# Kernel tuning notes

Hardware: AMD Instinct MI355X
Metric: run time of the kernel (lower is better)

Reference implementation:

```python
import jax, jax.numpy as jnp
import numpy as np

E, K, H, I = 16, 4, 2048, 1024
B, S = 1, 2048


def setup_inputs() -> dict:
    key = jax.random.key(0)
    ks = jax.random.split(key, 5)
    scale_in = 1.0 / np.sqrt(H)
    scale_mid = 1.0 / np.sqrt(I)
    return {
        "x": jax.random.normal(ks[0], (B, S, H), dtype=jnp.float32),
        "gate_w": jax.random.normal(ks[1], (E, H), dtype=jnp.float32) * scale_in,
        "w1_gate": jax.random.normal(ks[2], (E, I, H), dtype=jnp.float32) * scale_in,
        "w1_up": jax.random.normal(ks[3], (E, I, H), dtype=jnp.float32) * scale_in,
        "w2": jax.random.normal(ks[4], (E, H, I), dtype=jnp.float32) * scale_mid,
        "topk": K,
    }


def reference(x, gate_w, w1_gate, w1_up, w2, topk):
    orig_shape = x.shape
    xt = x.reshape(-1, x.shape[-1])            # [T, H]
    T = xt.shape[0]
    n_exp = gate_w.shape[0]

    # Router: top-k logits, softmax over the selected k (as in the torch code).
    logits = xt @ gate_w.T                      # [T, E]
    topk_vals, topk_ids = jax.lax.top_k(logits, topk)
    topk_w = jax.nn.softmax(topk_vals, axis=-1)  # [T, K]

    # Dense per-token-per-expert combine weight; 0 for unselected experts.
    # Mathematically identical to the gather/scatter-add loop: unselected
    # experts contribute expert_out * 0.
    gate_dense = jnp.zeros((T, n_exp), dtype=xt.dtype)
    gate_dense = gate_dense.at[jnp.arange(T)[:, None], topk_ids].add(topk_w)

    # SwiGLU per expert (dense over experts; weights zero-out unused ones).
    g = jnp.einsum("th,eih->tei", xt, w1_gate)   # [T, E, I]
    u = jnp.einsum("th,eih->tei", xt, w1_up)     # [T, E, I]
    h = jax.nn.silu(g) * u                        # [T, E, I]
    out = jnp.einsum("tei,te,ehi->th", h, gate_dense, w2)  # [T, H]
    return out.reshape(orig_shape)
```

## Files before the change

kernel.cpp:

```cpp
#include <hip/hip_runtime.h>
#include <hip/hip_bf16.h>
#include <stdint.h>

#define NEXP 16
#define KSEL 4
#define HDIM 2048
#define IDIM 1024
#define TTOK 2048
#define MAXTILES 80
#define NT1 16
#define NTB 16
#define MAXB1 (MAXTILES * NT1)
#define MAXBB (MAXTILES * NTB)
#define NCVT 1024
#define NW8 ((NEXP * IDIM * HDIM) / 8)

typedef __attribute__((ext_vector_type(8))) short bf16x8;
typedef __attribute__((ext_vector_type(4))) float f32x4;
typedef __attribute__((ext_vector_type(4))) unsigned int u32x4;
typedef unsigned int u32;

__device__ __forceinline__ uint32_t pack2(float a, float b) {
  __hip_bfloat162 h = __float22bfloat162_rn(float2{a, b});
  uint32_t u;
  __builtin_memcpy(&u, &h, 4);
  return u;
}
__device__ __forceinline__ ushort bf1(float a) {
  __hip_bfloat16 h = __float2bfloat16(a);
  ushort u;
  __builtin_memcpy(&u, &h, 2);
  return u;
}
__device__ __forceinline__ float bf2f(ushort u) {
  uint32_t v = (uint32_t)u << 16;
  float f;
  __builtin_memcpy(&f, &v, 4);
  return f;
}
__device__ __forceinline__ void gload16(const void* g, void* l) {
  __builtin_amdgcn_global_load_lds(
      (const __attribute__((address_space(1))) u32*)g,
      (__attribute__((address_space(3))) u32*)l, 16, 0, 0);
}
__device__ __forceinline__ int swzread(int row, int q) {
  return row * 32 + ((q ^ ((row >> 1) & 3)) << 3);
}
__device__ __forceinline__ void cvt_body(const float* __restrict__ src,
                                         ushort* __restrict__ dst,
                                         int blk, int nblk) {
  const int stride = nblk * 256;
  for (int i = blk * 256 + (int)threadIdx.x; i < NW8; i += stride) {
    f32x4 a = __builtin_nontemporal_load(((const f32x4*)src) + i * 2);
    f32x4 b = __builtin_nontemporal_load(((const f32x4*)src) + i * 2 + 1);
    uint4 t;
    t.x = pack2(a[0], a[1]); t.y = pack2(a[2], a[3]);
    t.z = pack2(b[0], b[1]); t.w = pack2(b[2], b[3]);
    ((uint4*)dst)[i] = t;
  }
}

__global__ __launch_bounds__(256) void router_kernel(
    const float* __restrict__ x, const float* __restrict__ gw,
    ushort* __restrict__ xb, int* __restrict__ topk_id,
    float* __restrict__ topk_w,
    const float* __restrict__ srcG, ushort* __restrict__ dstG,
    const float* __restrict__ srcU, ushort* __restrict__ dstU)
{
  if (blockIdx.x >= TTOK / 4 + NCVT) {
    cvt_body(srcU, dstU, blockIdx.x - (TTOK / 4 + NCVT), NCVT);
    return;
  }
  if (blockIdx.x >= TTOK / 4) {
    cvt_body(srcG, dstG, blockIdx.x - TTOK / 4, NCVT);
    return;
  }
  const int wid = threadIdx.x >> 6;
  const int lane = threadIdx.x & 63;
  const int t = blockIdx.x * 4 + wid;
  const float4* x4 = (const float4*)(x + (size_t)t * HDIM);
  const float4* gw4 = (const float4*)gw;
  float acc[NEXP];
#pragma unroll
  for (int e = 0; e < NEXP; ++e) acc[e] = 0.f;
#pragma unroll
  for (int i = 0; i < HDIM / 256; ++i) {
    const int idx = i * 64 + lane;
    float4 xv = x4[idx];
    uint2 xp;
    xp.x = pack2(xv.x, xv.y);
    xp.y = pack2(xv.z, xv.w);
    *(uint2*)(xb + (size_t)t * HDIM + idx * 4) = xp;
#pragma unroll
    for (int e = 0; e < NEXP; ++e) {
      float4 wv = gw4[e * (HDIM / 4) + idx];
      acc[e] += xv.x * wv.x + xv.y * wv.y + xv.z * wv.z + xv.w * wv.w;
    }
  }
#pragma unroll
  for (int e = 0; e < NEXP; ++e) {
#pragma unroll
    for (int off = 32; off >= 1; off >>= 1)
      acc[e] += __shfl_xor(acc[e], off);
  }
  if (lane == 0) {
    unsigned taken = 0;
    float vals[KSEL];
    int ids[KSEL];
#pragma unroll
    for (int k = 0; k < KSEL; ++k) {
      float bv = -3.4e38f; int bi = 0;
      for (int e = 0; e < NEXP; ++e)
        if (!((taken >> e) & 1u) && acc[e] > bv) { bv = acc[e]; bi = e; }
      taken |= 1u << bi; vals[k] = bv; ids[k] = bi;
    }
    float m = vals[0], s = 0.f, w[KSEL];
#pragma unroll
    for (int k = 0; k < KSEL; ++k) { w[k] = __expf(vals[k] - m); s += w[k]; }
    float is = 1.f / s;
#pragma unroll
    for (int k = 0; k < KSEL; ++k) {
      topk_id[t * KSEL + k] = ids[k];
      topk_w[t * KSEL + k] = w[k] * is;
    }
  }
}

__global__ __launch_bounds__(1024) void plan_scatter_kernel(
    const int* __restrict__ topk_id, int* __restrict__ counts,
    int* __restrict__ offsets, int* __restrict__ nWA, int* __restrict__ nWB,
    int* __restrict__ wlA, int* __restrict__ wlB,
    int* __restrict__ rowTok, int* __restrict__ inv)
{
  __shared__ int cnt[NEXP], off[NEXP], cur[NEXP], tiles[NEXP], pre[NEXP];
  const int tid = threadIdx.x;
  if (tid < NEXP) { cnt[tid] = 0; cur[tid] = 0; }
  __syncthreads();
  for (int i = tid; i < TTOK * KSEL; i += 1024)
    atomicAdd(&cnt[topk_id[i]], 1);
  __syncthreads();
  if (tid == 0) {
    int s = 0, p = 0;
    for (int e = 0; e < NEXP; ++e) {
      off[e] = s; s += cnt[e];
      tiles[e] = (cnt[e] + 127) >> 7;
      pre[e] = p; p += tiles[e];
    }
    *nWA = p * NT1;
    *nWB = p * NTB;
  }
  __syncthreads();
  if (tid < NEXP) {
    counts[tid] = cnt[tid];
    offsets[tid] = off[tid];
    const int e = tid, T = tiles[e];
    int idx = pre[e] * NT1;
    for (int nt = 0; nt < NT1; ++nt)
      for (int mt = 0; mt < T; ++mt)
        wlA[idx++] = (e << 12) | (nt << 6) | mt;
  } else if (tid < 2 * NEXP) {
    const int e = tid - NEXP, T = tiles[e];
    int idx = pre[e] * NTB;
    for (int nt = 0; nt < NTB; ++nt)
      for (int mt = 0; mt < T; ++mt)
        wlB[idx++] = (e << 12) | (nt << 6) | mt;
  }
  for (int i = tid; i < TTOK * KSEL; i += 1024) {
    const int e = topk_id[i];
    const int pos = atomicAdd(&cur[e], 1);
    const int row = off[e] + pos;
    rowTok[row] = i >> 2;
    inv[i] = row;
  }
}

__global__ __launch_bounds__(256) void gemm1_kernel(
    const ushort* __restrict__ xb,
    const ushort* __restrict__ wG, const ushort* __restrict__ wU,
    const int* __restrict__ rowTok, const int* __restrict__ counts,
    const int* __restrict__ offsets, const int* __restrict__ nW,
    const int* __restrict__ wl, ushort* __restrict__ hbuf,
    const float* __restrict__ cvsrc, ushort* __restrict__ cvdst)
{
  if (blockIdx.x >= MAXB1) {
    cvt_body(cvsrc, cvdst, blockIdx.x - MAXB1, NCVT);
    return;
  }
  const int nTot = *nW;
  const int L = (blockIdx.x & 7) * (MAXB1 / 8) + (blockIdx.x >> 3);
  if (L >= nTot) return;
  const int w = wl[L];
  const int e = w >> 12, nt = (w >> 6) & 63, mt = w & 63;
  const int n_e = counts[e], rowbase = offsets[e];

  __shared__ ushort As[2][128 * 32];
  __shared__ ushort Bg[2][64 * 32];
  __shared__ ushort Bu[2][64 * 32];

  const int tid = threadIdx.x;
  const int r0 = tid >> 2;
  const int ck = tid & 3;
  const int sch = (ck ^ ((r0 >> 1) & 3)) << 3;

  const int ar0 = mt * 128 + r0, ar1 = ar0 + 64;
  const int tok0 = rowTok[rowbase + (ar0 < n_e ? ar0 : n_e - 1)];
  const int tok1 = rowTok[rowbase + (ar1 < n_e ? ar1 : n_e - 1)];
  const ushort* pA0 = xb + (size_t)tok0 * HDIM + sch;
  const ushort* pA1 = xb + (size_t)tok1 * HDIM + sch;
  const size_t wbase = (size_t)e * IDIM * HDIM;
  const ushort* pBg = wG + wbase + (size_t)(nt * 64 + r0) * HDIM + sch;
  const ushort* pBu = wU + wbase + (size_t)(nt * 64 + r0) * HDIM + sch;

  const int lane = tid & 63;
  const int wid = tid >> 6;
  const int wr = (wid >> 1) << 6;
  const int wc = (wid & 1) << 5;
  const int lr = lane & 15;
  const int q = lane >> 4;

  f32x4 accG[4][2], accU[4][2];
#pragma unroll
  for (int i = 0; i < 4; ++i)
#pragma unroll
    for (int j = 0; j < 2; ++j) {
      accG[i][j] = (f32x4){0.f, 0.f, 0.f, 0.f};
      accU[i][j] = (f32x4){0.f, 0.f, 0.f, 0.f};
    }

  auto STAGE = [&](int b) {
    gload16(pA0, &As[b][tid * 8]);
    gload16(pA1, &As[b][2048 + tid * 8]);
    gload16(pBg, &Bg[b][tid * 8]);
    gload16(pBu, &Bu[b][tid * 8]);
    pA0 += 32; pA1 += 32; pBg += 32; pBu += 32;
  };

  const int NTK = HDIM / 32;
  STAGE(0);
  __syncthreads();
  int buf = 0;
  for (int kt = 0; kt < NTK; ++kt) {
    if (kt + 1 < NTK) STAGE(buf ^ 1);
    bf16x8 af[4], bg[2], bu[2];
#pragma unroll
    for (int mi = 0; mi < 4; ++mi)
      af[mi] = *(const bf16x8*)&As[buf][swzread(wr + mi * 16 + lr, q)];
#pragma unroll
    for (int ni = 0; ni < 2; ++ni) {
      bg[ni] = *(const bf16x8*)&Bg[buf][swzread(wc + ni * 16 + lr, q)];
      bu[ni] = *(const bf16x8*)&Bu[buf][swzread(wc + ni * 16 + lr, q)];
    }
#pragma unroll
    for (int mi = 0; mi < 4; ++mi)
#pragma unroll
      for (int ni = 0; ni < 2; ++ni) {
        accG[mi][ni] = __builtin_amdgcn_mfma_f32_16x16x32_bf16(af[mi], bg[ni], accG[mi][ni], 0, 0, 0);
        accU[mi][ni] = __builtin_amdgcn_mfma_f32_16x16x32_bf16(af[mi], bu[ni], accU[mi][ni], 0, 0, 0);
      }
    __syncthreads();
    buf ^= 1;
  }

#pragma unroll
  for (int mi = 0; mi < 4; ++mi) {
#pragma unroll
    for (int ni = 0; ni < 2; ++ni) {
      const int col = nt * 64 + wc + ni * 16 + lr;
#pragma unroll
      for (int r = 0; r < 4; ++r) {
        const int mrow = mt * 128 + wr + mi * 16 + q * 4 + r;
        if (mrow < n_e) {
          const float gv = accG[mi][ni][r];
          const float uv = accU[mi][ni][r];
          const float hv = (gv / (1.f + __expf(-gv))) * uv;
          hbuf[(size_t)(rowbase + mrow) * IDIM + col] = bf1(hv);
        }
      }
    }
  }
}

__global__ __launch_bounds__(256) void gemmB_kernel(
    const ushort* __restrict__ hb, const ushort* __restrict__ wb,
    const int* __restrict__ counts, const int* __restrict__ offsets,
    const int* __restrict__ nW, const int* __restrict__ wl,
    ushort* __restrict__ po)
{
  const int nTot = *nW;
  const int L = (blockIdx.x & 7) * (MAXBB / 8) + (blockIdx.x >> 3);
  if (L >= nTot) return;
  const int w = wl[L];
  const int e = w >> 12, nt = (w >> 6) & 63, mt = w & 63;
  const int n_e = counts[e], rowbase = offsets[e];

  __shared__ ushort As[2][128 * 32];
  __shared__ ushort Bs[2][128 * 32];

  const int tid = threadIdx.x;
  const int r0 = tid >> 2;
  const int ck = tid & 3;
  const int sch = (ck ^ ((r0 >> 1) & 3)) << 3;

  const int ar0 = mt * 128 + r0, ar1 = ar0 + 64;
  const int g0 = rowbase + (ar0 < n_e ? ar0 : n_e - 1);
  const int g1 = rowbase + (ar1 < n_e ? ar1 : n_e - 1);
  const ushort* pA0 = hb + (size_t)g0 * IDIM + sch;
  const ushort* pA1 = hb + (size_t)g1 * IDIM + sch;
  const size_t wbase = (size_t)e * HDIM * IDIM;
  const ushort* pB0 = wb + wbase + (size_t)(nt * 128 + r0) * IDIM + sch;
  const ushort* pB1 = wb + wbase + (size_t)(nt * 128 + r0 + 64) * IDIM + sch;

  const int lane = tid & 63;
  const int wid = tid >> 6;
  const int wr = (wid >> 1) << 6;
  const int wc = (wid & 1) << 6;
  const int lr = lane & 15;
  const int q = lane >> 4;

  f32x4 acc[4][4];
#pragma unroll
  for (int i = 0; i < 4; ++i)
#pragma unroll
    for (int j = 0; j < 4; ++j) acc[i][j] = (f32x4){0.f, 0.f, 0.f, 0.f};

  auto STAGE = [&](int b) {
    gload16(pA0, &As[b][tid * 8]);
    gload16(pA1, &As[b][2048 + tid * 8]);
    gload16(pB0, &Bs[b][tid * 8]);
    gload16(pB1, &Bs[b][2048 + tid * 8]);
    pA0 += 32; pA1 += 32; pB0 += 32; pB1 += 32;
  };

  const int NTK = IDIM / 32;
  STAGE(0);
  __syncthreads();
  int buf = 0;
  for (int kt = 0; kt < NTK; ++kt) {
    if (kt + 1 < NTK) STAGE(buf ^ 1);
    bf16x8 af[4], bfr[4];
#pragma unroll
    for (int mi = 0; mi < 4; ++mi)
      af[mi] = *(const bf16x8*)&As[buf][swzread(wr + mi * 16 + lr, q)];
#pragma unroll
    for (int ni = 0; ni < 4; ++ni)
      bfr[ni] = *(const bf16x8*)&Bs[buf][swzread(wc + ni * 16 + lr, q)];
#pragma unroll
    for (int mi = 0; mi < 4; ++mi)
#pragma unroll
      for (int ni = 0; ni < 4; ++ni)
        acc[mi][ni] = __builtin_amdgcn_mfma_f32_16x16x32_bf16(af[mi], bfr[ni], acc[mi][ni], 0, 0, 0);
    __syncthreads();
    buf ^= 1;
  }

#pragma unroll
  for (int mi = 0; mi < 4; ++mi) {
#pragma unroll
    for (int ni = 0; ni < 4; ++ni) {
      const int col = nt * 128 + wc + ni * 16 + lr;
#pragma unroll
      for (int r = 0; r < 4; ++r) {
        const int mrow = mt * 128 + wr + mi * 16 + q * 4 + r;
        if (mrow < n_e)
          po[(size_t)(rowbase + mrow) * HDIM + col] = bf1(acc[mi][ni][r]);
      }
    }
  }
}

__global__ __launch_bounds__(256) void combine_kernel(
    const ushort* __restrict__ po, const int* __restrict__ inv,
    const float* __restrict__ tw, float* __restrict__ out)
{
  const int t = blockIdx.x;
  const int r0 = inv[t * 4 + 0], r1 = inv[t * 4 + 1];
  const int r2 = inv[t * 4 + 2], r3 = inv[t * 4 + 3];
  const float w0 = tw[t * 4 + 0], w1 = tw[t * 4 + 1];
  const float w2v = tw[t * 4 + 2], w3 = tw[t * 4 + 3];
  const int i = threadIdx.x;
  uint4 v0 = *(const uint4*)(po + (size_t)r0 * HDIM + i * 8);
  uint4 v1 = *(const uint4*)(po + (size_t)r1 * HDIM + i * 8);
  uint4 v2 = *(const uint4*)(po + (size_t)r2 * HDIM + i * 8);
  uint4 v3 = *(const uint4*)(po + (size_t)r3 * HDIM + i * 8);
  float o[8];
#pragma unroll
  for (int w = 0; w < 4; ++w) {
    const uint32_t a = (&v0.x)[w], b = (&v1.x)[w], c = (&v2.x)[w], d = (&v3.x)[w];
    o[w * 2 + 0] = w0 * __builtin_bit_cast(float, a << 16) +
                   w1 * __builtin_bit_cast(float, b << 16) +
                   w2v * __builtin_bit_cast(float, c << 16) +
                   w3 * __builtin_bit_cast(float, d << 16);
    o[w * 2 + 1] = w0 * __builtin_bit_cast(float, a & 0xffff0000u) +
                   w1 * __builtin_bit_cast(float, b & 0xffff0000u) +
                   w2v * __builtin_bit_cast(float, c & 0xffff0000u) +
                   w3 * __builtin_bit_cast(float, d & 0xffff0000u);
  }
  float4* o4 = (float4*)(out + (size_t)t * HDIM + i * 8);
  o4[0] = (float4){o[0], o[1], o[2], o[3]};
  o4[1] = (float4){o[4], o[5], o[6], o[7]};
}

extern "C" void kernel_launch(void* const* d_in, const int* in_sizes, int n_in,
                              void* d_out, int out_size, void* d_ws, size_t ws_size,
                              hipStream_t stream) {
  const float* x   = (const float*)d_in[0];
  const float* gw  = (const float*)d_in[1];
  const float* w1g = (const float*)d_in[2];
  const float* w1u = (const float*)d_in[3];
  const float* w2  = (const float*)d_in[4];
  float* out = (float*)d_out;

  char* ws = (char*)d_ws;
  ushort* xb    = (ushort*)(ws + 0);
  ushort* wbufG = (ushort*)(ws + 8388608);
  ushort* wbufU = (ushort*)(ws + 75497472);
  ushort* wbuf2 = (ushort*)(ws + 142606336);
  ushort* hbuf  = (ushort*)(ws + 209715200);
  ushort* po    = (ushort*)(ws + 226492416);
  int*    tkid   = (int*)(ws + 260046848);
  float*  tkw    = (float*)(ws + 260046848 + 32768);
  int*    rowTok = (int*)(ws + 260046848 + 65536);
  int*    inv    = (int*)(ws + 260046848 + 98304);
  int*    ctrl   = (int*)(ws + 260177920);
  int* counts  = ctrl;
  int* offsets = ctrl + 32;
  int* nWA     = ctrl + 50;
  int* nWB     = ctrl + 51;
  int* wlA     = ctrl + 64;
  int* wlB     = ctrl + 64 + MAXB1;

  router_kernel<<<TTOK / 4 + 2 * NCVT, 256, 0, stream>>>(
      x, gw, xb, tkid, tkw, w1g, wbufG, w1u, wbufU);
  plan_scatter_kernel<<<1, 1024, 0, stream>>>(tkid, counts, offsets, nWA, nWB,
                                              wlA, wlB, rowTok, inv);
  gemm1_kernel<<<MAXB1 + NCVT, 256, 0, stream>>>(
      xb, wbufG, wbufU, rowTok, counts, offsets, nWA, wlA, hbuf,
      w2, wbuf2);
  gemmB_kernel<<<MAXBB, 256, 0, stream>>>(hbuf, wbuf2, counts, offsets,
                                          nWB, wlB, po);
  combine_kernel<<<TTOK, 256, 0, stream>>>(po, inv, tkw, out);
}
```

Baseline: 326.3 us.

## Double gemm1 M-tile to 256 rows with 512-thread blocks

gemm1 now processes 256 routed rows per block instead of 128, using 8 waves. Each wave stages 32 rows of activations, and the expert weight loads are split so four waves fetch the gate rows and four fetch the up rows. The plan kernel builds separate tile counts for gemm1 and gemmB, and the weight-conversion helper is generalised to take an explicit start index and stride. Larger M tiles halve how often each expert's weight tile is re-read, at the cost of more padding waste on partial tiles, fewer blocks, and higher LDS use per block.

```diff
diff --git a/kernel.cpp b/kernel.cpp
--- a/kernel.cpp
+++ b/kernel.cpp
@@ -7,17 +7,18 @@
 #define HDIM 2048
 #define IDIM 1024
 #define TTOK 2048
-#define MAXTILES 80
 #define NT1 16
 #define NTB 16
-#define MAXB1 (MAXTILES * NT1)
-#define MAXBB (MAXTILES * NTB)
+#define MAXT1 47
+#define MAXB1 (MAXT1 * NT1)
+#define MAXTB 80
+#define MAXBB (MAXTB * NTB)
 #define NCVT 1024
+#define NCVT1 512
 #define NW8 ((NEXP * IDIM * HDIM) / 8)
 
 typedef __attribute__((ext_vector_type(8))) short bf16x8;
 typedef __attribute__((ext_vector_type(4))) float f32x4;
-typedef __attribute__((ext_vector_type(4))) unsigned int u32x4;
 typedef unsigned int u32;
 
 __device__ __forceinline__ uint32_t pack2(float a, float b) {
@@ -32,12 +33,6 @@
   __builtin_memcpy(&u, &h, 2);
   return u;
 }
-__device__ __forceinline__ float bf2f(ushort u) {
-  uint32_t v = (uint32_t)u << 16;
-  float f;
-  __builtin_memcpy(&f, &v, 4);
-  return f;
-}
 __device__ __forceinline__ void gload16(const void* g, void* l) {
   __builtin_amdgcn_global_load_lds(
       (const __attribute__((address_space(1))) u32*)g,
@@ -46,11 +41,10 @@
 __device__ __forceinline__ int swzread(int row, int q) {
   return row * 32 + ((q ^ ((row >> 1) & 3)) << 3);
 }
-__device__ __forceinline__ void cvt_body(const float* __restrict__ src,
-                                         ushort* __restrict__ dst,
-                                         int blk, int nblk) {
-  const int stride = nblk * 256;
-  for (int i = blk * 256 + (int)threadIdx.x; i < NW8; i += stride) {
+__device__ __forceinline__ void cvt_bodyN(const float* __restrict__ src,
+                                          ushort* __restrict__ dst,
+                                          int idx0, int stride) {
+  for (int i = idx0; i < NW8; i += stride) {
     f32x4 a = __builtin_nontemporal_load(((const f32x4*)src) + i * 2);
     f32x4 b = __builtin_nontemporal_load(((const f32x4*)src) + i * 2 + 1);
     uint4 t;
@@ -68,11 +62,13 @@
     const float* __restrict__ srcU, ushort* __restrict__ dstU)
 {
   if (blockIdx.x >= TTOK / 4 + NCVT) {
-    cvt_body(srcU, dstU, blockIdx.x - (TTOK / 4 + NCVT), NCVT);
+    cvt_bodyN(srcU, dstU,
+              (blockIdx.x - (TTOK / 4 + NCVT)) * 256 + threadIdx.x, NCVT * 256);
     return;
   }
   if (blockIdx.x >= TTOK / 4) {
-    cvt_body(srcG, dstG, blockIdx.x - TTOK / 4, NCVT);
+    cvt_bodyN(srcG, dstG,
+              (blockIdx.x - TTOK / 4) * 256 + threadIdx.x, NCVT * 256);
     return;
   }
   const int wid = threadIdx.x >> 6;
@@ -132,7 +128,8 @@
     int* __restrict__ wlA, int* __restrict__ wlB,
     int* __restrict__ rowTok, int* __restrict__ inv)
 {
-  __shared__ int cnt[NEXP], off[NEXP], cur[NEXP], tiles[NEXP], pre[NEXP];
+  __shared__ int cnt[NEXP], off[NEXP], cur[NEXP];
+  __shared__ int t1[NEXP], p1[NEXP], tB[NEXP], pB[NEXP];
   const int tid = threadIdx.x;
   if (tid < NEXP) { cnt[tid] = 0; cur[tid] = 0; }
   __syncthreads();
@@ -140,27 +137,27 @@
     atomicAdd(&cnt[topk_id[i]], 1);
   __syncthreads();
   if (tid == 0) {
-    int s = 0, p = 0;
+    int s = 0, a = 0, b = 0;
     for (int e = 0; e < NEXP; ++e) {
       off[e] = s; s += cnt[e];
-      tiles[e] = (cnt[e] + 127) >> 7;
-      pre[e] = p; p += tiles[e];
-    }
-    *nWA = p * NT1;
-    *nWB = p * NTB;
+      t1[e] = (cnt[e] + 255) >> 8;  p1[e] = a;  a += t1[e];
+      tB[e] = (cnt[e] + 127) >> 7;  pB[e] = b;  b += tB[e];
+    }
+    *nWA = a * NT1;
+    *nWB = b * NTB;
   }
   __syncthreads();
   if (tid < NEXP) {
     counts[tid] = cnt[tid];
     offsets[tid] = off[tid];
-    const int e = tid, T = tiles[e];
-    int idx = pre[e] * NT1;
+    const int e = tid, T = t1[e];
+    int idx = p1[e] * NT1;
     for (int nt = 0; nt < NT1; ++nt)
       for (int mt = 0; mt < T; ++mt)
         wlA[idx++] = (e << 12) | (nt << 6) | mt;
   } else if (tid < 2 * NEXP) {
-    const int e = tid - NEXP, T = tiles[e];
-    int idx = pre[e] * NTB;
+    const int e = tid - NEXP, T = tB[e];
+    int idx = pB[e] * NTB;
     for (int nt = 0; nt < NTB; ++nt)
       for (int mt = 0; mt < T; ++mt)
         wlB[idx++] = (e << 12) | (nt << 6) | mt;
@@ -174,7 +171,7 @@
   }
 }
 
-__global__ __launch_bounds__(256) void gemm1_kernel(
+__global__ __launch_bounds__(512) void gemm1_kernel(
     const ushort* __restrict__ xb,
     const ushort* __restrict__ wG, const ushort* __restrict__ wU,
     const int* __restrict__ rowTok, const int* __restrict__ counts,
@@ -183,7 +180,8 @@
     const float* __restrict__ cvsrc, ushort* __restrict__ cvdst)
 {
   if (blockIdx.x >= MAXB1) {
-    cvt_body(cvsrc, cvdst, blockIdx.x - MAXB1, NCVT);
+    cvt_bodyN(cvsrc, cvdst,
+              (blockIdx.x - MAXB1) * 512 + threadIdx.x, NCVT1 * 512);
     return;
   }
   const int nTot = *nW;
@@ -193,26 +191,31 @@
   const int e = w >> 12, nt = (w >> 6) & 63, mt = w & 63;
   const int n_e = counts[e], rowbase = offsets[e];
 
-  __shared__ ushort As[2][128 * 32];
+  __shared__ ushort As[2][256 * 32];
   __shared__ ushort Bg[2][64 * 32];
   __shared__ ushort Bu[2][64 * 32];
 
   const int tid = threadIdx.x;
-  const int r0 = tid >> 2;
-  const int ck = tid & 3;
-  const int sch = (ck ^ ((r0 >> 1) & 3)) << 3;
-
-  const int ar0 = mt * 128 + r0, ar1 = ar0 + 64;
-  const int tok0 = rowTok[rowbase + (ar0 < n_e ? ar0 : n_e - 1)];
-  const int tok1 = rowTok[rowbase + (ar1 < n_e ? ar1 : n_e - 1)];
-  const ushort* pA0 = xb + (size_t)tok0 * HDIM + sch;
-  const ushort* pA1 = xb + (size_t)tok1 * HDIM + sch;
-  const size_t wbase = (size_t)e * IDIM * HDIM;
-  const ushort* pBg = wG + wbase + (size_t)(nt * 64 + r0) * HDIM + sch;
-  const ushort* pBu = wU + wbase + (size_t)(nt * 64 + r0) * HDIM + sch;
-
   const int lane = tid & 63;
   const int wid = tid >> 6;
+
+  const int lr4 = lane >> 2;
+  const int ckA = lane & 3;
+  const int arl0 = wid * 32 + lr4;
+  const int arl1 = wid * 32 + 16 + lr4;
+  const int schA0 = (ckA ^ ((arl0 >> 1) & 3)) << 3;
+  const int schA1 = (ckA ^ ((arl1 >> 1) & 3)) << 3;
+  const int ag0 = mt * 256 + arl0, ag1 = mt * 256 + arl1;
+  const int tok0 = rowTok[rowbase + (ag0 < n_e ? ag0 : n_e - 1)];
+  const int tok1 = rowTok[rowbase + (ag1 < n_e ? ag1 : n_e - 1)];
+  const ushort* pA0 = xb + (size_t)tok0 * HDIM + schA0;
+  const ushort* pA1 = xb + (size_t)tok1 * HDIM + schA1;
+  const int brl = (wid & 3) * 16 + lr4;
+  const int schB = (ckA ^ ((brl >> 1) & 3)) << 3;
+  const size_t wbase = (size_t)e * IDIM * HDIM;
+  const ushort* pB = ((wid < 4) ? wG : wU) + wbase +
+                     (size_t)(nt * 64 + brl) * HDIM + schB;
+
   const int wr = (wid >> 1) << 6;
   const int wc = (wid & 1) << 5;
   const int lr = lane & 15;
@@ -228,11 +231,11 @@
     }
 
   auto STAGE = [&](int b) {
-    gload16(pA0, &As[b][tid * 8]);
-    gload16(pA1, &As[b][2048 + tid * 8]);
-    gload16(pBg, &Bg[b][tid * 8]);
-    gload16(pBu, &Bu[b][tid * 8]);
-    pA0 += 32; pA1 += 32; pBg += 32; pBu += 32;
+    gload16(pA0, &As[b][wid * 1024 + lane * 8]);
+    gload16(pA1, &As[b][wid * 1024 + 512 + lane * 8]);
+    if (wid < 4) gload16(pB, &Bg[b][wid * 512 + lane * 8]);
+    else         gload16(pB, &Bu[b][(wid - 4) * 512 + lane * 8]);
+    pA0 += 32; pA1 += 32; pB += 32;
   };
 
   const int NTK = HDIM / 32;
@@ -268,7 +271,7 @@
       const int col = nt * 64 + wc + ni * 16 + lr;
 #pragma unroll
       for (int r = 0; r < 4; ++r) {
-        const int mrow = mt * 128 + wr + mi * 16 + q * 4 + r;
+        const int mrow = mt * 256 + wr + mi * 16 + q * 4 + r;
         if (mrow < n_e) {
           const float gv = accG[mi][ni][r];
           const float uv = accU[mi][ni][r];
@@ -433,7 +436,7 @@
       x, gw, xb, tkid, tkw, w1g, wbufG, w1u, wbufU);
   plan_scatter_kernel<<<1, 1024, 0, stream>>>(tkid, counts, offsets, nWA, nWB,
                                               wlA, wlB, rowTok, inv);
-  gemm1_kernel<<<MAXB1 + NCVT, 256, 0, stream>>>(
+  gemm1_kernel<<<MAXB1 + NCVT1, 512, 0, stream>>>(
       xb, wbufG, wbufU, rowTok, counts, offsets, nWA, wlA, hbuf,
       w2, wbuf2);
   gemmB_kernel<<<MAXBB, 256, 0, stream>>>(hbuf, wbuf2, counts, offsets,
```

New measurement: 312.6 us. 1.04x faster.
